# Performance work log

Measured on AMD Instinct MI355X. Metric: run time of the kernel, lower is better.

## Reference

```python
import jax, jax.numpy as jnp
import numpy as np

NUM_TREES = 150
ARITY = 4
DEPTH = 4
NUM_LEVELS = DEPTH + 1  # leaves (level 0) ... root (level DEPTH)
VOCAB = 10000
SUBTOK = 8
EMB_DIM = 256
HID = 256
NUM_CLASSES = 2


def _build_forest():
    # perfect ARITY-ary tree, level-order indexing; edges point child -> parent
    n = (ARITY ** (DEPTH + 1) - 1) // (ARITY - 1)  # 341
    src = np.arange(1, n)
    dst = (src - 1) // ARITY
    depth_of = np.zeros(n, dtype=np.int64)
    for j in range(1, n):
        depth_of[j] = depth_of[(j - 1) // ARITY] + 1
    level_of = DEPTH - depth_of  # leaves = 0, processed first (topo order)
    offs = np.arange(NUM_TREES) * n
    edge_src = (src[None, :] + offs[:, None]).ravel().astype(np.int32)
    edge_dst = (dst[None, :] + offs[:, None]).ravel().astype(np.int32)
    node_level = np.tile(level_of, NUM_TREES).astype(np.int32)
    graph_id = np.repeat(np.arange(NUM_TREES), n).astype(np.int32)
    leaf_mask = (node_level == 0).astype(np.int32)
    return edge_src, edge_dst, node_level, graph_id, leaf_mask, NUM_TREES * n


def setup_inputs() -> dict:
    key = jax.random.key(0)
    ks = jax.random.split(key, 16)
    es, ed, lvl, gid, lm, N = _build_forest()
    s_e = 1.0 / np.sqrt(EMB_DIM)
    s_h = 1.0 / np.sqrt(HID)
    s_f = 1.0 / np.sqrt(2 * HID)
    return {
        "node_feat1": jax.random.randint(ks[0], (N, SUBTOK), 0, VOCAB, dtype=jnp.int32),
        "node_feat2": jax.random.randint(ks[1], (N, SUBTOK), 0, VOCAB, dtype=jnp.int32),
        "emb1": jax.random.normal(ks[2], (VOCAB, EMB_DIM), jnp.float32) * 0.02,
        "emb2": jax.random.normal(ks[3], (VOCAB, EMB_DIM), jnp.float32) * 0.02,
        "W_iou1": jax.random.normal(ks[4], (EMB_DIM, 3 * HID), jnp.float32) * s_e,
        "W_iou2": jax.random.normal(ks[5], (EMB_DIM, 3 * HID), jnp.float32) * s_e,
        "U_iou1": jax.random.normal(ks[6], (HID, 3 * HID), jnp.float32) * s_h,
        "U_iou2": jax.random.normal(ks[7], (HID, 3 * HID), jnp.float32) * s_h,
        "Uf_W1": jax.random.normal(ks[8], (HID, HID), jnp.float32) * s_h,
        "Uf_b1": jnp.zeros((HID,), jnp.float32),
        "Uf_W2": jax.random.normal(ks[9], (HID, HID), jnp.float32) * s_h,
        "Uf_b2": jnp.zeros((HID,), jnp.float32),
        "b_iou1": jnp.zeros((3 * HID,), jnp.float32),
        "b_iou2": jnp.zeros((3 * HID,), jnp.float32),
        "Wf": jax.random.normal(ks[10], (2 * HID, NUM_CLASSES), jnp.float32) * s_f,
        "bf": jnp.zeros((NUM_CLASSES,), jnp.float32),
        "edge_src": jnp.asarray(es),
        "edge_dst": jnp.asarray(ed),
        "node_level": jnp.asarray(lvl),
        "graph_id": jnp.asarray(gid),
        "leaf_mask": jnp.asarray(lm),
    }


def _tree_lstm(iou0, U_iou, Uf_W, Uf_b, b_iou, edge_src, edge_dst, node_level):
    # ChildSum TreeLSTM, propagated level-by-level (leaves -> root)
    N = iou0.shape[0]
    h = jnp.zeros((N, HID), iou0.dtype)
    c = jnp.zeros((N, HID), iou0.dtype)
    for lvl in range(NUM_LEVELS):
        emask = (node_level[edge_dst] == lvl).astype(h.dtype)[:, None]  # [E,1]
        hs = h[edge_src] * emask  # children h (already computed at lower levels)
        f = jax.nn.sigmoid(hs @ Uf_W + Uf_b)  # per-edge forget gate
        h_tild = jax.ops.segment_sum(hs, edge_dst, num_segments=N)
        c_sum = jax.ops.segment_sum(f * c[edge_src] * emask, edge_dst, num_segments=N)
        has_child = jax.ops.segment_sum(emask, edge_dst, num_segments=N) > 0  # [N,1]
        # DGL semantics: reduce overwrites iou for internal nodes; leaves keep W_iou(x)*mask
        iou = jnp.where(has_child, h_tild @ U_iou, iou0) + b_iou
        i, o, u = jnp.split(iou, 3, axis=1)
        c_new = jax.nn.sigmoid(i) * jnp.tanh(u) + c_sum
        h_new = jax.nn.sigmoid(o) * jnp.tanh(c_new)
        at = (node_level == lvl)[:, None]
        h = jnp.where(at, h_new, h)
        c = jnp.where(at, c_new, c)
    return h


def _branch(node_feat, emb, W_iou, U_iou, Uf_W, Uf_b, b_iou,
            leaf_mask, edge_src, edge_dst, node_level, graph_id):
    embeds = emb[node_feat].mean(axis=1)  # subtoken mean pooling -> [N, EMB_DIM]
    iou0 = (embeds @ W_iou) * leaf_mask.astype(embeds.dtype)[:, None]
    h = _tree_lstm(iou0, U_iou, Uf_W, Uf_b, b_iou, edge_src, edge_dst, node_level)
    s = jax.ops.segment_sum(h, graph_id, num_segments=NUM_TREES)
    cnt = jax.ops.segment_sum(jnp.ones((h.shape[0],), h.dtype), graph_id, num_segments=NUM_TREES)
    return jax.nn.relu(s / cnt[:, None])  # mean graph readout + relu


def reference(node_feat1, node_feat2, emb1, emb2, W_iou1, W_iou2, U_iou1, U_iou2,
              Uf_W1, Uf_b1, Uf_W2, Uf_b2, b_iou1, b_iou2, Wf, bf,
              edge_src, edge_dst, node_level, graph_id, leaf_mask):
    m1 = _branch(node_feat1, emb1, W_iou1, U_iou1, Uf_W1, Uf_b1, b_iou1,
                 leaf_mask, edge_src, edge_dst, node_level, graph_id)
    m2 = _branch(node_feat2, emb2, W_iou2, U_iou2, Uf_W2, Uf_b2, b_iou2,
                 leaf_mask, edge_src, edge_dst, node_level, graph_id)
    logits = jax.nn.leaky_relu(jnp.concatenate([m1, m2], axis=1) @ Wf + bf, 0.01)
    return jax.nn.softmax(logits, axis=-1)
```

## Files before the change

### kernel.cpp

```cpp
#include <hip/hip_runtime.h>

#define NT 150
#define NPT 341
#define VOCAB 10000

typedef __attribute__((ext_vector_type(8))) short short8;
typedef __attribute__((ext_vector_type(4))) float floatx4;

__device__ __forceinline__ float sigf(float x){ return 1.0f/(1.0f+__expf(-x)); }
__device__ __forceinline__ float bf2f(ushort u){ union{unsigned i; float f;} v; v.i = ((unsigned)u)<<16; return v.f; }
__device__ __forceinline__ ushort f2bf(float x){ union{float f; unsigned i;} v; v.f = x; return (ushort)((v.i + 0x7fff + ((v.i>>16)&1))>>16); }

__global__ __launch_bounds__(256) void convW_k(
    const float* __restrict__ W1, const float* __restrict__ U1, const float* __restrict__ F1,
    const float* __restrict__ W2, const float* __restrict__ U2, const float* __restrict__ F2,
    ushort* Wt1, ushort* Ut1, ushort* Ft1, ushort* Wt2, ushort* Ut2, ushort* Ft2){
  __shared__ float T[32][33];
  const float* src; ushort* dst; int N;
  switch (blockIdx.z){
    case 0: src=W1; dst=Wt1; N=768; break;
    case 1: src=U1; dst=Ut1; N=768; break;
    case 2: src=F1; dst=Ft1; N=256; break;
    case 3: src=W2; dst=Wt2; N=768; break;
    case 4: src=U2; dst=Ut2; N=768; break;
    default: src=F2; dst=Ft2; N=256; break;
  }
  int n0 = blockIdx.x*32; if (n0 >= N) return;
  int k0 = blockIdx.y*32;
  int nl = threadIdx.x & 31, kb = threadIdx.x >> 5;
  #pragma unroll
  for (int i=0;i<4;i++){ int kk = kb*4+i; T[kk][nl] = src[(size_t)(k0+kk)*N + n0 + nl]; }
  __syncthreads();
  #pragma unroll
  for (int i=0;i<4;i++){ int nn = kb*4+i; dst[(size_t)(n0+nn)*256 + k0 + nl] = f2bf(T[nl][nn]); }
}

__global__ __launch_bounds__(256) void convE_k(
    const float* __restrict__ e1, const float* __restrict__ e2,
    ushort* __restrict__ E1, ushort* __restrict__ E2){
  const float* s = blockIdx.y ? e2 : e1;
  ushort* d = blockIdx.y ? E2 : E1;
  size_t i = ((size_t)blockIdx.x*256 + threadIdx.x)*4;
  float4 v = *(const float4*)&s[i];
  d[i+0]=f2bf(v.x); d[i+1]=f2bf(v.y); d[i+2]=f2bf(v.z); d[i+3]=f2bf(v.w);
}

__global__ __launch_bounds__(1024) void subtree_k(
    const int* __restrict__ f1, const int* __restrict__ f2,
    const ushort* __restrict__ E1, const ushort* __restrict__ E2,
    const ushort* __restrict__ Wt1, const float* __restrict__ b1,
    const ushort* __restrict__ Ut1, const ushort* __restrict__ Ft1, const float* __restrict__ Ufb1,
    const ushort* __restrict__ Wt2, const float* __restrict__ b2,
    const ushort* __restrict__ Ut2, const ushort* __restrict__ Ft2, const float* __restrict__ Ufb2,
    ushort* __restrict__ h1, ushort* __restrict__ c1,
    ushort* __restrict__ h2, ushort* __restrict__ c2,
    float* __restrict__ part){
  __shared__ __attribute__((aligned(16))) ushort As[8][64*40];
  __shared__ __attribute__((aligned(16))) ushort Ht[8][16*40];
  __shared__ float Csum[16][272];
  int br = blockIdx.y;
  const int* feat = br ? f2 : f1;
  const ushort* E = br ? E2 : E1;
  const ushort* Wt = br ? Wt2 : Wt1;
  const float* biou = br ? b2 : b1;
  const ushort* Ut = br ? Ut2 : Ut1;
  const ushort* Ft = br ? Ft2 : Ft1;
  const float* Ufb = br ? Ufb2 : Ufb1;
  ushort* h = br ? h2 : h1;
  ushort* c = br ? c2 : c1;
  int s = blockIdx.x;
  int tree = s >> 2, j = s & 3;
  size_t nbase = (size_t)tree*NPT;
  int tid = threadIdx.x, lane = tid & 63, wav = tid >> 6, quad = lane >> 4, l15 = lane & 15;

  {
    int row = tid >> 4, seg = tid & 15;
    size_t node = nbase + 85 + 64*j + row;
    const int* f = feat + node*8;
    float sm[16];
    #pragma unroll
    for (int q=0;q<16;q++) sm[q]=0.f;
    #pragma unroll
    for (int t8=0;t8<8;t8++){
      const ushort* rp = E + (size_t)f[t8]*256 + seg*16;
      short8 a = *(const short8*)rp;
      short8 b = *(const short8*)(rp+8);
      #pragma unroll
      for (int q=0;q<8;q++){ sm[q]+=bf2f((ushort)a[q]); sm[8+q]+=bf2f((ushort)b[q]); }
    }
    short8 o1, o2;
    #pragma unroll
    for (int q=0;q<8;q++){ o1[q]=(short)f2bf(sm[q]*0.125f); o2[q]=(short)f2bf(sm[8+q]*0.125f); }
    int cch = seg >> 1, off = (seg & 1)*16;
    *(short8*)&As[cch][row*40 + off]     = o1;
    *(short8*)&As[cch][row*40 + off + 8] = o2;
  }
  __syncthreads();

  int hcol = wav*16 + l15;
  int cch = hcol >> 5, coff = hcol & 31;
  float bi = biou[hcol], bo = biou[256+hcol], bu = biou[512+hcol];

  floatx4 acc[3][4];
  #pragma unroll
  for (int g=0;g<3;g++)
    #pragma unroll
    for (int r=0;r<4;r++) acc[g][r] = (floatx4){0.f,0.f,0.f,0.f};
  {
    const ushort* bp0 = Wt + (size_t)(0*256 + hcol)*256 + quad*8;
    const ushort* bp1 = Wt + (size_t)(1*256 + hcol)*256 + quad*8;
    const ushort* bp2 = Wt + (size_t)(2*256 + hcol)*256 + quad*8;
    #pragma unroll
    for (int k8=0;k8<8;k8++){
      short8 b0 = *(const short8*)(bp0 + k8*32);
      short8 b1 = *(const short8*)(bp1 + k8*32);
      short8 b2 = *(const short8*)(bp2 + k8*32);
      #pragma unroll
      for (int r=0;r<4;r++){
        short8 a = *(const short8*)&As[k8][(16*r + l15)*40 + quad*8];
        acc[0][r] = __builtin_amdgcn_mfma_f32_16x16x32_bf16(a, b0, acc[0][r], 0,0,0);
        acc[1][r] = __builtin_amdgcn_mfma_f32_16x16x32_bf16(a, b1, acc[1][r], 0,0,0);
        acc[2][r] = __builtin_amdgcn_mfma_f32_16x16x32_bf16(a, b2, acc[2][r], 0,0,0);
      }
    }
  }
  float hL[4][4], cL[4][4], htd[4];
  #pragma unroll
  for (int r=0;r<4;r++){
    htd[r] = 0.f;
    #pragma unroll
    for (int reg=0;reg<4;reg++){
      float iv = acc[0][r][reg] + bi;
      float ov = acc[1][r][reg] + bo;
      float uv = acc[2][r][reg] + bu;
      float cc_ = sigf(iv)*tanhf(uv);
      float hh = sigf(ov)*tanhf(cc_);
      cL[r][reg] = cc_; hL[r][reg] = hh; htd[r] += hh;
    }
  }
  __syncthreads();
  float sA = 0.f;
  #pragma unroll
  for (int r=0;r<4;r++){
    #pragma unroll
    for (int reg=0;reg<4;reg++){
      As[cch][(16*r + quad*4 + reg)*40 + coff] = f2bf(hL[r][reg]);
      sA += hL[r][reg];
    }
    Ht[cch][(4*r + quad)*40 + coff] = f2bf(htd[r]);
  }
  __syncthreads();

  floatx4 af[4], ai, ao, au;
  #pragma unroll
  for (int r=0;r<4;r++) af[r] = (floatx4){0.f,0.f,0.f,0.f};
  ai = (floatx4){0.f,0.f,0.f,0.f}; ao = ai; au = ai;
  {
    const ushort* bfp = Ft + (size_t)hcol*256 + quad*8;
    const ushort* up0 = Ut + (size_t)(0*256 + hcol)*256 + quad*8;
    const ushort* up1 = Ut + (size_t)(256 + hcol)*256 + quad*8;
    const ushort* up2 = Ut + (size_t)(512 + hcol)*256 + quad*8;
    #pragma unroll
    for (int k8=0;k8<8;k8++){
      short8 Bf = *(const short8*)(bfp + k8*32);
      short8 B0 = *(const short8*)(up0 + k8*32);
      short8 B1 = *(const short8*)(up1 + k8*32);
      short8 B2 = *(const short8*)(up2 + k8*32);
      short8 ah = *(const short8*)&Ht[k8][l15*40 + quad*8];
      #pragma unroll
      for (int r=0;r<4;r++){
        short8 a = *(const short8*)&As[k8][(16*r + l15)*40 + quad*8];
        af[r] = __builtin_amdgcn_mfma_f32_16x16x32_bf16(a, Bf, af[r], 0,0,0);
      }
      ai = __builtin_amdgcn_mfma_f32_16x16x32_bf16(ah, B0, ai, 0,0,0);
      ao = __builtin_amdgcn_mfma_f32_16x16x32_bf16(ah, B1, ao, 0,0,0);
      au = __builtin_amdgcn_mfma_f32_16x16x32_bf16(ah, B2, au, 0,0,0);
    }
  }
  float ufb = Ufb[hcol];
  #pragma unroll
  for (int r=0;r<4;r++){
    float cs = 0.f;
    #pragma unroll
    for (int reg=0;reg<4;reg++) cs += sigf(af[r][reg] + ufb) * cL[r][reg];
    Csum[4*r + quad][hcol] = cs;
  }
  #pragma unroll
  for (int reg=0;reg<4;reg++){
    int p = quad*4 + reg;
    float cs = Csum[p][hcol];
    float iv = ai[reg] + bi, ov = ao[reg] + bo, uv = au[reg] + bu;
    float cn = sigf(iv)*tanhf(uv) + cs;
    float hn = sigf(ov)*tanhf(cn);
    sA += hn;
    size_t off = (nbase + 21 + 16*j + p)*256 + hcol;
    h[off] = f2bf(hn);
    c[off] = f2bf(cn);
  }
  sA += __shfl_xor(sA, 16);
  sA += __shfl_xor(sA, 32);
  if (quad == 0) part[((size_t)(s*2 + br))*256 + hcol] = sA;
}

__global__ __launch_bounds__(1024) void upper_k(
    const ushort* __restrict__ Ut1, const ushort* __restrict__ Ft1,
    const float* __restrict__ Ufb1, const float* __restrict__ b1,
    const ushort* __restrict__ Ut2, const ushort* __restrict__ Ft2,
    const float* __restrict__ Ufb2, const float* __restrict__ b2,
    const ushort* __restrict__ h1, const ushort* __restrict__ c1,
    const ushort* __restrict__ h2, const ushort* __restrict__ c2,
    const float* __restrict__ part, const float* __restrict__ Wf,
    const float* __restrict__ bfv, float* __restrict__ out){
  __shared__ __attribute__((aligned(16))) ushort As[8][64*40];
  __shared__ __attribute__((aligned(16))) ushort Ht[8][16*40];
  __shared__ float Csum[16][272];
  __shared__ float Ms[2][256];
  __shared__ float red[32];
  int tree = blockIdx.x;
  size_t nbase = (size_t)tree*NPT;
  int tid = threadIdx.x, lane = tid & 63, wav = tid >> 6, quad = lane >> 4, l15 = lane & 15;
  int hcol = wav*16 + l15;
  int cch = hcol >> 5, coff = hcol & 31;

  for (int br=0; br<2; br++){
    const ushort* Ut = br ? Ut2 : Ut1;
    const ushort* Ft = br ? Ft2 : Ft1;
    const float* Ufb = br ? Ufb2 : Ufb1;
    const float* biou = br ? b2 : b1;
    const ushort* h = br ? h2 : h1;
    const ushort* c = br ? c2 : c1;
    float bi = biou[hcol], bo = biou[256+hcol], bu = biou[512+hcol];
    float ufb = Ufb[hcol];

    {
      int row = tid >> 4, seg = tid & 15;
      const ushort* src = h + (nbase + 21 + row)*256 + seg*16;
      short8 a = *(const short8*)src;
      short8 b = *(const short8*)(src+8);
      int cc2 = seg >> 1, off = (seg & 1)*16;
      *(short8*)&As[cc2][row*40 + off]     = a;
      *(short8*)&As[cc2][row*40 + off + 8] = b;
    }
    float cL0[4][4];
    #pragma unroll
    for (int r=0;r<4;r++)
      #pragma unroll
      for (int reg=0;reg<4;reg++)
        cL0[r][reg] = bf2f(c[(nbase + 21 + 16*r + quad*4 + reg)*256 + hcol]);
    __syncthreads();
    if (tid < 512){
      int n = tid >> 5, sg = tid & 31;
      int cc2 = sg >> 2, off = (sg & 3)*8;
      float s8[8];
      #pragma unroll
      for (int q=0;q<8;q++) s8[q]=0.f;
      #pragma unroll
      for (int i=0;i<4;i++){
        short8 v = *(const short8*)&As[cc2][(4*n+i)*40 + off];
        #pragma unroll
        for (int q=0;q<8;q++) s8[q] += bf2f((ushort)v[q]);
      }
      short8 o;
      #pragma unroll
      for (int q=0;q<8;q++) o[q] = (short)f2bf(s8[q]);
      *(short8*)&Ht[cc2][n*40 + off] = o;
    }
    __syncthreads();

    const ushort* bfp = Ft + (size_t)hcol*256 + quad*8;
    const ushort* up0 = Ut + (size_t)(0*256 + hcol)*256 + quad*8;
    const ushort* up1 = Ut + (size_t)(256 + hcol)*256 + quad*8;
    const ushort* up2 = Ut + (size_t)(512 + hcol)*256 + quad*8;

    floatx4 af1[4], ai1, ao1, au1;
    #pragma unroll
    for (int r=0;r<4;r++) af1[r] = (floatx4){0.f,0.f,0.f,0.f};
    ai1 = (floatx4){0.f,0.f,0.f,0.f}; ao1 = ai1; au1 = ai1;
    #pragma unroll
    for (int k8=0;k8<8;k8++){
      short8 Bf = *(const short8*)(bfp + k8*32);
      short8 B0 = *(const short8*)(up0 + k8*32);
      short8 B1 = *(const short8*)(up1 + k8*32);
      short8 B2 = *(const short8*)(up2 + k8*32);
      short8 ah = *(const short8*)&Ht[k8][l15*40 + quad*8];
      #pragma unroll
      for (int r=0;r<4;r++){
        short8 a = *(const short8*)&As[k8][(16*r + l15)*40 + quad*8];
        af1[r] = __builtin_amdgcn_mfma_f32_16x16x32_bf16(a, Bf, af1[r], 0,0,0);
      }
      ai1 = __builtin_amdgcn_mfma_f32_16x16x32_bf16(ah, B0, ai1, 0,0,0);
      ao1 = __builtin_amdgcn_mfma_f32_16x16x32_bf16(ah, B1, ao1, 0,0,0);
      au1 = __builtin_amdgcn_mfma_f32_16x16x32_bf16(ah, B2, au1, 0,0,0);
    }
    #pragma unroll
    for (int r=0;r<4;r++){
      float cs = 0.f;
      #pragma unroll
      for (int reg=0;reg<4;reg++) cs += sigf(af1[r][reg] + ufb) * cL0[r][reg];
      Csum[4*r + quad][hcol] = cs;
    }
    float h1v[4], c1v[4], sB = 0.f;
    #pragma unroll
    for (int reg=0;reg<4;reg++){
      int p = quad*4 + reg;
      float cs = Csum[p][hcol];
      float iv = ai1[reg]+bi, ov = ao1[reg]+bo, uv = au1[reg]+bu;
      c1v[reg] = sigf(iv)*tanhf(uv) + cs;
      h1v[reg] = sigf(ov)*tanhf(c1v[reg]);
      sB += h1v[reg];
    }
    __syncthreads();
    #pragma unroll
    for (int reg=0;reg<4;reg++)
      Ht[cch][(quad*4 + reg)*40 + coff] = f2bf(h1v[reg]);
    __syncthreads();

    floatx4 af2, ai2, ao2, au2;
    af2 = (floatx4){0.f,0.f,0.f,0.f}; ai2 = af2; ao2 = af2; au2 = af2;
    #pragma unroll
    for (int k8=0;k8<8;k8++){
      short8 Bf = *(const short8*)(bfp + k8*32);
      short8 B0 = *(const short8*)(up0 + k8*32);
      short8 B1 = *(const short8*)(up1 + k8*32);
      short8 B2 = *(const short8*)(up2 + k8*32);
      short8 a = *(const short8*)&Ht[k8][l15*40 + quad*8];
      af2 = __builtin_amdgcn_mfma_f32_16x16x32_bf16(a, Bf, af2, 0,0,0);
      ai2 = __builtin_amdgcn_mfma_f32_16x16x32_bf16(a, B0, ai2, 0,0,0);
      ao2 = __builtin_amdgcn_mfma_f32_16x16x32_bf16(a, B1, ao2, 0,0,0);
      au2 = __builtin_amdgcn_mfma_f32_16x16x32_bf16(a, B2, au2, 0,0,0);
    }
    float cs2 = 0.f;
    #pragma unroll
    for (int reg=0;reg<4;reg++) cs2 += sigf(af2[reg] + ufb) * c1v[reg];
    float iv2 = ai2[0]+ai2[1]+ai2[2]+ai2[3] + bi;
    float ov2 = ao2[0]+ao2[1]+ao2[2]+ao2[3] + bo;
    float uv2 = au2[0]+au2[1]+au2[2]+au2[3] + bu;
    float c2v = sigf(iv2)*tanhf(uv2) + cs2;
    float h2v = sigf(ov2)*tanhf(c2v);
    sB += h2v;
    __syncthreads();
    Ht[cch][quad*40 + coff] = f2bf(h2v);
    #pragma unroll
    for (int z=1;z<4;z++) Ht[cch][(quad + 4*z)*40 + coff] = 0;
    __syncthreads();

    floatx4 af3, ai3, ao3, au3;
    af3 = (floatx4){0.f,0.f,0.f,0.f}; ai3 = af3; ao3 = af3; au3 = af3;
    #pragma unroll
    for (int k8=0;k8<8;k8++){
      short8 Bf = *(const short8*)(bfp + k8*32);
      short8 B0 = *(const short8*)(up0 + k8*32);
      short8 B1 = *(const short8*)(up1 + k8*32);
      short8 B2 = *(const short8*)(up2 + k8*32);
      short8 a = *(const short8*)&Ht[k8][l15*40 + quad*8];
      af3 = __builtin_amdgcn_mfma_f32_16x16x32_bf16(a, Bf, af3, 0,0,0);
      ai3 = __builtin_amdgcn_mfma_f32_16x16x32_bf16(a, B0, ai3, 0,0,0);
      ao3 = __builtin_amdgcn_mfma_f32_16x16x32_bf16(a, B1, ao3, 0,0,0);
      au3 = __builtin_amdgcn_mfma_f32_16x16x32_bf16(a, B2, au3, 0,0,0);
    }
    float c2c[4];
    #pragma unroll
    for (int reg=0;reg<4;reg++) c2c[reg] = __shfl(c2v, reg*16 + l15);
    {
      float cs3 = 0.f;
      #pragma unroll
      for (int reg=0;reg<4;reg++) cs3 += sigf(af3[reg] + ufb) * c2c[reg];
      float iv3 = ai3[0]+ai3[1]+ai3[2]+ai3[3] + bi;
      float ov3 = ao3[0]+ao3[1]+ao3[2]+ao3[3] + bo;
      float uv3 = au3[0]+au3[1]+au3[2]+au3[3] + bu;
      float c3 = sigf(iv3)*tanhf(uv3) + cs3;
      float hr = sigf(ov3)*tanhf(c3);
      if (quad == 0) sB += hr;
    }
    sB += __shfl_xor(sB, 16);
    sB += __shfl_xor(sB, 32);
    if (quad == 0){
      float tot = sB;
      #pragma unroll
      for (int jj=0;jj<4;jj++)
        tot += part[((size_t)((tree*4 + jj)*2 + br))*256 + hcol];
      Ms[br][hcol] = fmaxf(tot*(1.0f/341.0f), 0.f);
    }
    __syncthreads();
  }

  float p0 = 0.f, p1 = 0.f;
  if (tid < 512){
    float x = Ms[tid >> 8][tid & 255];
    p0 = x*Wf[tid*2+0]; p1 = x*Wf[tid*2+1];
  }
  #pragma unroll
  for (int off=32; off>0; off>>=1){
    p0 += __shfl_down(p0, off);
    p1 += __shfl_down(p1, off);
  }
  if (lane == 0){ red[wav] = p0; red[16+wav] = p1; }
  __syncthreads();
  if (tid == 0){
    float l0 = bfv[0], l1 = bfv[1];
    #pragma unroll
    for (int w=0;w<16;w++){ l0 += red[w]; l1 += red[16+w]; }
    l0 = (l0>0.f)?l0:0.01f*l0;
    l1 = (l1>0.f)?l1:0.01f*l1;
    float mx = fmaxf(l0,l1);
    float e0 = __expf(l0-mx), e1 = __expf(l1-mx);
    float inv = 1.0f/(e0+e1);
    out[tree*2+0] = e0*inv; out[tree*2+1] = e1*inv;
  }
}

extern "C" void kernel_launch(void* const* d_in, const int* in_sizes, int n_in,
                              void* d_out, int out_size, void* d_ws, size_t ws_size,
                              hipStream_t stream) {
  const int*   feat1 = (const int*)  d_in[0];
  const int*   feat2 = (const int*)  d_in[1];
  const float* emb1  = (const float*)d_in[2];
  const float* emb2  = (const float*)d_in[3];
  const float* Wiou1 = (const float*)d_in[4];
  const float* Wiou2 = (const float*)d_in[5];
  const float* Uiou1 = (const float*)d_in[6];
  const float* Uiou2 = (const float*)d_in[7];
  const float* UfW1  = (const float*)d_in[8];
  const float* Ufb1  = (const float*)d_in[9];
  const float* UfW2  = (const float*)d_in[10];
  const float* Ufb2  = (const float*)d_in[11];
  const float* biou1 = (const float*)d_in[12];
  const float* biou2 = (const float*)d_in[13];
  const float* Wf    = (const float*)d_in[14];
  const float* bfv   = (const float*)d_in[15];
  float* out = (float*)d_out;

  char* ws = (char*)d_ws;
  ushort* h1  = (ushort*)ws;  ws += (size_t)NT*NPT*256*2;
  ushort* h2  = (ushort*)ws;  ws += (size_t)NT*NPT*256*2;
  ushort* c1  = (ushort*)ws;  ws += (size_t)NT*NPT*256*2;
  ushort* c2  = (ushort*)ws;  ws += (size_t)NT*NPT*256*2;
  ushort* E1  = (ushort*)ws;  ws += (size_t)VOCAB*256*2;
  ushort* E2  = (ushort*)ws;  ws += (size_t)VOCAB*256*2;
  ushort* Wt1 = (ushort*)ws;  ws += 768*256*2;
  ushort* Ut1 = (ushort*)ws;  ws += 768*256*2;
  ushort* Ft1 = (ushort*)ws;  ws += 256*256*2;
  ushort* Wt2 = (ushort*)ws;  ws += 768*256*2;
  ushort* Ut2 = (ushort*)ws;  ws += 768*256*2;
  ushort* Ft2 = (ushort*)ws;  ws += 256*256*2;
  float*  part = (float*)ws;  ws += (size_t)600*2*256*4;

  convE_k<<<dim3(2500, 2), 256, 0, stream>>>(emb1, emb2, E1, E2);
  convW_k<<<dim3(24, 8, 6), 256, 0, stream>>>(Wiou1, Uiou1, UfW1, Wiou2, Uiou2, UfW2,
                                              Wt1, Ut1, Ft1, Wt2, Ut2, Ft2);
  subtree_k<<<dim3(600, 2), 1024, 0, stream>>>(feat1, feat2, E1, E2,
                                               Wt1, biou1, Ut1, Ft1, Ufb1,
                                               Wt2, biou2, Ut2, Ft2, Ufb2,
                                               h1, c1, h2, c2, part);
  upper_k<<<NT, 1024, 0, stream>>>(Ut1, Ft1, Ufb1, biou1,
                                   Ut2, Ft2, Ufb2, biou2,
                                   h1, c1, h2, c2, part, Wf, bfv, out);
}
```

Measured before the change: 388.9 us.

## Store embedding tables as scaled FP8 and split upper kernel per branch

Embedding tables are now converted to scaled e4m3 FP8 instead of bf16, which halves the bytes moved by the conversion and by the subtoken gather. Separately, the upper-level kernel now runs one block per (tree, branch) instead of looping over both branches, which doubles its parallelism. The classifier head moves into a small final kernel, and subtree blocks interleave the two branches in a 1D grid. FP8 storage lowers embedding precision, and the extra launch adds a small fixed cost.

```diff
diff --git a/kernel.cpp b/kernel.cpp
--- a/kernel.cpp
+++ b/kernel.cpp
@@ -10,6 +10,38 @@
 __device__ __forceinline__ float sigf(float x){ return 1.0f/(1.0f+__expf(-x)); }
 __device__ __forceinline__ float bf2f(ushort u){ union{unsigned i; float f;} v; v.i = ((unsigned)u)<<16; return v.f; }
 __device__ __forceinline__ ushort f2bf(float x){ union{float f; unsigned i;} v; v.f = x; return (ushort)((v.i + 0x7fff + ((v.i>>16)&1))>>16); }
+
+__device__ unsigned char f2e4m3(float x){
+  float a = fabsf(x);
+  unsigned s = (x < 0.f) ? 1u : 0u;
+  if (a != a) return (unsigned char)((s<<7)|0x7f);
+  a = fminf(a, 448.f);
+  unsigned E, M;
+  if (a < 7.8125e-3f){
+    M = (unsigned)rintf(a*512.f); E = 0;
+    if (M > 7){ E = 1; M = 0; }
+  } else {
+    int e; float m = frexpf(a, &e);
+    if (e + 6 <= 0){
+      M = (unsigned)rintf(a*512.f); E = 0;
+      if (M > 7){ E = 1; M = 0; }
+    } else {
+      E = (unsigned)(e + 6);
+      M = (unsigned)rintf((m*2.f - 1.f)*8.f);
+      if (M > 7){ M = 0; E++; }
+      if (E > 15){ E = 15; M = 6; }
+    }
+  }
+  return (unsigned char)((s<<7)|(E<<3)|M);
+}
+
+__device__ __forceinline__ float fp8d(unsigned b){
+  unsigned e = (b>>3)&15u, m = b&7u, t = (e==0u) ? 1u : 0u;
+  union{unsigned u; float f;} w;
+  w.u = ((e + 120u + t)<<23) | (m<<20);
+  float mag = w.f - (t ? 0.015625f : 0.f);
+  return (b & 0x80u) ? -mag : mag;
+}
 
 __global__ __launch_bounds__(256) void convW_k(
     const float* __restrict__ W1, const float* __restrict__ U1, const float* __restrict__ F1,
@@ -37,17 +69,20 @@
 
 __global__ __launch_bounds__(256) void convE_k(
     const float* __restrict__ e1, const float* __restrict__ e2,
-    ushort* __restrict__ E1, ushort* __restrict__ E2){
+    unsigned char* __restrict__ E1, unsigned char* __restrict__ E2){
   const float* s = blockIdx.y ? e2 : e1;
-  ushort* d = blockIdx.y ? E2 : E1;
+  unsigned char* d = blockIdx.y ? E2 : E1;
   size_t i = ((size_t)blockIdx.x*256 + threadIdx.x)*4;
   float4 v = *(const float4*)&s[i];
-  d[i+0]=f2bf(v.x); d[i+1]=f2bf(v.y); d[i+2]=f2bf(v.z); d[i+3]=f2bf(v.w);
+  uchar4 o;
+  o.x = f2e4m3(v.x*64.f); o.y = f2e4m3(v.y*64.f);
+  o.z = f2e4m3(v.z*64.f); o.w = f2e4m3(v.w*64.f);
+  *(uchar4*)&d[i] = o;
 }
 
 __global__ __launch_bounds__(1024) void subtree_k(
     const int* __restrict__ f1, const int* __restrict__ f2,
-    const ushort* __restrict__ E1, const ushort* __restrict__ E2,
+    const unsigned char* __restrict__ E1, const unsigned char* __restrict__ E2,
     const ushort* __restrict__ Wt1, const float* __restrict__ b1,
     const ushort* __restrict__ Ut1, const ushort* __restrict__ Ft1, const float* __restrict__ Ufb1,
     const ushort* __restrict__ Wt2, const float* __restrict__ b2,
@@ -58,9 +93,11 @@
   __shared__ __attribute__((aligned(16))) ushort As[8][64*40];
   __shared__ __attribute__((aligned(16))) ushort Ht[8][16*40];
   __shared__ float Csum[16][272];
-  int br = blockIdx.y;
+  int bid = blockIdx.x;
+  int br = bid & 1;
+  int s = bid >> 1;
   const int* feat = br ? f2 : f1;
-  const ushort* E = br ? E2 : E1;
+  const unsigned char* E = br ? E2 : E1;
   const ushort* Wt = br ? Wt2 : Wt1;
   const float* biou = br ? b2 : b1;
   const ushort* Ut = br ? Ut2 : Ut1;
@@ -68,7 +105,6 @@
   const float* Ufb = br ? Ufb2 : Ufb1;
   ushort* h = br ? h2 : h1;
   ushort* c = br ? c2 : c1;
-  int s = blockIdx.x;
   int tree = s >> 2, j = s & 3;
   size_t nbase = (size_t)tree*NPT;
   int tid = threadIdx.x, lane = tid & 63, wav = tid >> 6, quad = lane >> 4, l15 = lane & 15;
@@ -82,15 +118,20 @@
     for (int q=0;q<16;q++) sm[q]=0.f;
     #pragma unroll
     for (int t8=0;t8<8;t8++){
-      const ushort* rp = E + (size_t)f[t8]*256 + seg*16;
-      short8 a = *(const short8*)rp;
-      short8 b = *(const short8*)(rp+8);
+      uint4 rv = *(const uint4*)(E + (size_t)f[t8]*256 + seg*16);
+      unsigned wd[4] = {rv.x, rv.y, rv.z, rv.w};
       #pragma unroll
-      for (int q=0;q<8;q++){ sm[q]+=bf2f((ushort)a[q]); sm[8+q]+=bf2f((ushort)b[q]); }
+      for (int w=0;w<4;w++)
+        #pragma unroll
+        for (int b8=0;b8<4;b8++)
+          sm[w*4+b8] += fp8d((wd[w]>>(8*b8)) & 0xffu);
     }
     short8 o1, o2;
     #pragma unroll
-    for (int q=0;q<8;q++){ o1[q]=(short)f2bf(sm[q]*0.125f); o2[q]=(short)f2bf(sm[8+q]*0.125f); }
+    for (int q=0;q<8;q++){
+      o1[q]=(short)f2bf(sm[q]*0.001953125f);
+      o2[q]=(short)f2bf(sm[8+q]*0.001953125f);
+    }
     int cch = seg >> 1, off = (seg & 1)*16;
     *(short8*)&As[cch][row*40 + off]     = o1;
     *(short8*)&As[cch][row*40 + off + 8] = o2;
@@ -209,197 +250,195 @@
     const float* __restrict__ Ufb2, const float* __restrict__ b2,
     const ushort* __restrict__ h1, const ushort* __restrict__ c1,
     const ushort* __restrict__ h2, const ushort* __restrict__ c2,
-    const float* __restrict__ part, const float* __restrict__ Wf,
-    const float* __restrict__ bfv, float* __restrict__ out){
+    const float* __restrict__ part,
+    float* __restrict__ m1, float* __restrict__ m2){
   __shared__ __attribute__((aligned(16))) ushort As[8][64*40];
   __shared__ __attribute__((aligned(16))) ushort Ht[8][16*40];
   __shared__ float Csum[16][272];
-  __shared__ float Ms[2][256];
-  __shared__ float red[32];
-  int tree = blockIdx.x;
+  int bid = blockIdx.x;
+  int br = bid & 1;
+  int tree = bid >> 1;
+  const ushort* Ut = br ? Ut2 : Ut1;
+  const ushort* Ft = br ? Ft2 : Ft1;
+  const float* Ufb = br ? Ufb2 : Ufb1;
+  const float* biou = br ? b2 : b1;
+  const ushort* h = br ? h2 : h1;
+  const ushort* c = br ? c2 : c1;
+  float* mo = br ? m2 : m1;
   size_t nbase = (size_t)tree*NPT;
   int tid = threadIdx.x, lane = tid & 63, wav = tid >> 6, quad = lane >> 4, l15 = lane & 15;
   int hcol = wav*16 + l15;
   int cch = hcol >> 5, coff = hcol & 31;
-
-  for (int br=0; br<2; br++){
-    const ushort* Ut = br ? Ut2 : Ut1;
-    const ushort* Ft = br ? Ft2 : Ft1;
-    const float* Ufb = br ? Ufb2 : Ufb1;
-    const float* biou = br ? b2 : b1;
-    const ushort* h = br ? h2 : h1;
-    const ushort* c = br ? c2 : c1;
-    float bi = biou[hcol], bo = biou[256+hcol], bu = biou[512+hcol];
-    float ufb = Ufb[hcol];
-
-    {
-      int row = tid >> 4, seg = tid & 15;
-      const ushort* src = h + (nbase + 21 + row)*256 + seg*16;
-      short8 a = *(const short8*)src;
-      short8 b = *(const short8*)(src+8);
-      int cc2 = seg >> 1, off = (seg & 1)*16;
-      *(short8*)&As[cc2][row*40 + off]     = a;
-      *(short8*)&As[cc2][row*40 + off + 8] = b;
-    }
-    float cL0[4][4];
-    #pragma unroll
-    for (int r=0;r<4;r++)
+  float bi = biou[hcol], bo = biou[256+hcol], bu = biou[512+hcol];
+  float ufb = Ufb[hcol];
+
+  {
+    int row = tid >> 4, seg = tid & 15;
+    const ushort* src = h + (nbase + 21 + row)*256 + seg*16;
+    short8 a = *(const short8*)src;
+    short8 b = *(const short8*)(src+8);
+    int cc2 = seg >> 1, off = (seg & 1)*16;
+    *(short8*)&As[cc2][row*40 + off]     = a;
+    *(short8*)&As[cc2][row*40 + off + 8] = b;
+  }
+  float cL0[4][4];
+  #pragma unroll
+  for (int r=0;r<4;r++)
+    #pragma unroll
+    for (int reg=0;reg<4;reg++)
+      cL0[r][reg] = bf2f(c[(nbase + 21 + 16*r + quad*4 + reg)*256 + hcol]);
+  __syncthreads();
+  if (tid < 512){
+    int n = tid >> 5, sg = tid & 31;
+    int cc2 = sg >> 2, off = (sg & 3)*8;
+    float s8[8];
+    #pragma unroll
+    for (int q=0;q<8;q++) s8[q]=0.f;
+    #pragma unroll
+    for (int i=0;i<4;i++){
+      short8 v = *(const short8*)&As[cc2][(4*n+i)*40 + off];
       #pragma unroll
-      for (int reg=0;reg<4;reg++)
-        cL0[r][reg] = bf2f(c[(nbase + 21 + 16*r + quad*4 + reg)*256 + hcol]);
-    __syncthreads();
-    if (tid < 512){
-      int n = tid >> 5, sg = tid & 31;
-      int cc2 = sg >> 2, off = (sg & 3)*8;
-      float s8[8];
-      #pragma unroll
-      for (int q=0;q<8;q++) s8[q]=0.f;
-      #pragma unroll
-      for (int i=0;i<4;i++){
-        short8 v = *(const short8*)&As[cc2][(4*n+i)*40 + off];
-        #pragma unroll
-        for (int q=0;q<8;q++) s8[q] += bf2f((ushort)v[q]);
-      }
-      short8 o;
-      #pragma unroll
-      for (int q=0;q<8;q++) o[q] = (short)f2bf(s8[q]);
-      *(short8*)&Ht[cc2][n*40 + off] = o;
-    }
-    __syncthreads();
-
-    const ushort* bfp = Ft + (size_t)hcol*256 + quad*8;
-    const ushort* up0 = Ut + (size_t)(0*256 + hcol)*256 + quad*8;
-    const ushort* up1 = Ut + (size_t)(256 + hcol)*256 + quad*8;
-    const ushort* up2 = Ut + (size_t)(512 + hcol)*256 + quad*8;
-
-    floatx4 af1[4], ai1, ao1, au1;
-    #pragma unroll
-    for (int r=0;r<4;r++) af1[r] = (floatx4){0.f,0.f,0.f,0.f};
-    ai1 = (floatx4){0.f,0.f,0.f,0.f}; ao1 = ai1; au1 = ai1;
-    #pragma unroll
-    for (int k8=0;k8<8;k8++){
-      short8 Bf = *(const short8*)(bfp + k8*32);
-      short8 B0 = *(const short8*)(up0 + k8*32);
-      short8 B1 = *(const short8*)(up1 + k8*32);
-      short8 B2 = *(const short8*)(up2 + k8*32);
-      short8 ah = *(const short8*)&Ht[k8][l15*40 + quad*8];
-      #pragma unroll
-      for (int r=0;r<4;r++){
-        short8 a = *(const short8*)&As[k8][(16*r + l15)*40 + quad*8];
-        af1[r] = __builtin_amdgcn_mfma_f32_16x16x32_bf16(a, Bf, af1[r], 0,0,0);
-      }
-      ai1 = __builtin_amdgcn_mfma_f32_16x16x32_bf16(ah, B0, ai1, 0,0,0);
-      ao1 = __builtin_amdgcn_mfma_f32_16x16x32_bf16(ah, B1, ao1, 0,0,0);
-      au1 = __builtin_amdgcn_mfma_f32_16x16x32_bf16(ah, B2, au1, 0,0,0);
-    }
+      for (int q=0;q<8;q++) s8[q] += bf2f((ushort)v[q]);
+    }
+    short8 o;
+    #pragma unroll
+    for (int q=0;q<8;q++) o[q] = (short)f2bf(s8[q]);
+    *(short8*)&Ht[cc2][n*40 + off] = o;
+  }
+  __syncthreads();
+
+  const ushort* bfp = Ft + (size_t)hcol*256 + quad*8;
+  const ushort* up0 = Ut + (size_t)(0*256 + hcol)*256 + quad*8;
+  const ushort* up1 = Ut + (size_t)(256 + hcol)*256 + quad*8;
+  const ushort* up2 = Ut + (size_t)(512 + hcol)*256 + quad*8;
+
+  floatx4 af1[4], ai1, ao1, au1;
+  #pragma unroll
+  for (int r=0;r<4;r++) af1[r] = (floatx4){0.f,0.f,0.f,0.f};
+  ai1 = (floatx4){0.f,0.f,0.f,0.f}; ao1 = ai1; au1 = ai1;
+  #pragma unroll
+  for (int k8=0;k8<8;k8++){
+    short8 Bf = *(const short8*)(bfp + k8*32);
+    short8 B0 = *(const short8*)(up0 + k8*32);
+    short8 B1 = *(const short8*)(up1 + k8*32);
+    short8 B2 = *(const short8*)(up2 + k8*32);
+    short8 ah = *(const short8*)&Ht[k8][l15*40 + quad*8];
     #pragma unroll
     for (int r=0;r<4;r++){
-      float cs = 0.f;
-      #pragma unroll
-      for (int reg=0;reg<4;reg++) cs += sigf(af1[r][reg] + ufb) * cL0[r][reg];
-      Csum[4*r + quad][hcol] = cs;
-    }
-    float h1v[4], c1v[4], sB = 0.f;
-    #pragma unroll
-    for (int reg=0;reg<4;reg++){
-      int p = quad*4 + reg;
-      float cs = Csum[p][hcol];
-      float iv = ai1[reg]+bi, ov = ao1[reg]+bo, uv = au1[reg]+bu;
-      c1v[reg] = sigf(iv)*tanhf(uv) + cs;
-      h1v[reg] = sigf(ov)*tanhf(c1v[reg]);
-      sB += h1v[reg];
-    }
-    __syncthreads();
-    #pragma unroll
-    for (int reg=0;reg<4;reg++)
-      Ht[cch][(quad*4 + reg)*40 + coff] = f2bf(h1v[reg]);
-    __syncthreads();
-
-    floatx4 af2, ai2, ao2, au2;
-    af2 = (floatx4){0.f,0.f,0.f,0.f}; ai2 = af2; ao2 = af2; au2 = af2;
-    #pragma unroll
-    for (int k8=0;k8<8;k8++){
-      short8 Bf = *(const short8*)(bfp + k8*32);
-      short8 B0 = *(const short8*)(up0 + k8*32);
-      short8 B1 = *(const short8*)(up1 + k8*32);
-      short8 B2 = *(const short8*)(up2 + k8*32);
-      short8 a = *(const short8*)&Ht[k8][l15*40 + quad*8];
-      af2 = __builtin_amdgcn_mfma_f32_16x16x32_bf16(a, Bf, af2, 0,0,0);
-      ai2 = __builtin_amdgcn_mfma_f32_16x16x32_bf16(a, B0, ai2, 0,0,0);
-      ao2 = __builtin_amdgcn_mfma_f32_16x16x32_bf16(a, B1, ao2, 0,0,0);
-      au2 = __builtin_amdgcn_mfma_f32_16x16x32_bf16(a, B2, au2, 0,0,0);
-    }
-    float cs2 = 0.f;
-    #pragma unroll
-    for (int reg=0;reg<4;reg++) cs2 += sigf(af2[reg] + ufb) * c1v[reg];
-    float iv2 = ai2[0]+ai2[1]+ai2[2]+ai2[3] + bi;
-    float ov2 = ao2[0]+ao2[1]+ao2[2]+ao2[3] + bo;
-    float uv2 = au2[0]+au2[1]+au2[2]+au2[3] + bu;
-    float c2v = sigf(iv2)*tanhf(uv2) + cs2;
-    float h2v = sigf(ov2)*tanhf(c2v);
-    sB += h2v;
-    __syncthreads();
-    Ht[cch][quad*40 + coff] = f2bf(h2v);
-    #pragma unroll
-    for (int z=1;z<4;z++) Ht[cch][(quad + 4*z)*40 + coff] = 0;
-    __syncthreads();
-
-    floatx4 af3, ai3, ao3, au3;
-    af3 = (floatx4){0.f,0.f,0.f,0.f}; ai3 = af3; ao3 = af3; au3 = af3;
-    #pragma unroll
-    for (int k8=0;k8<8;k8++){
-      short8 Bf = *(const short8*)(bfp + k8*32);
-      short8 B0 = *(const short8*)(up0 + k8*32);
-      short8 B1 = *(const short8*)(up1 + k8*32);
-      short8 B2 = *(const short8*)(up2 + k8*32);
-      short8 a = *(const short8*)&Ht[k8][l15*40 + quad*8];
-      af3 = __builtin_amdgcn_mfma_f32_16x16x32_bf16(a, Bf, af3, 0,0,0);
-      ai3 = __builtin_amdgcn_mfma_f32_16x16x32_bf16(a, B0, ai3, 0,0,0);
-      ao3 = __builtin_amdgcn_mfma_f32_16x16x32_bf16(a, B1, ao3, 0,0,0);
-      au3 = __builtin_amdgcn_mfma_f32_16x16x32_bf16(a, B2, au3, 0,0,0);
-    }
-    float c2c[4];
-    #pragma unroll
-    for (int reg=0;reg<4;reg++) c2c[reg] = __shfl(c2v, reg*16 + l15);
-    {
-      float cs3 = 0.f;
-      #pragma unroll
-      for (int reg=0;reg<4;reg++) cs3 += sigf(af3[reg] + ufb) * c2c[reg];
-      float iv3 = ai3[0]+ai3[1]+ai3[2]+ai3[3] + bi;
-      float ov3 = ao3[0]+ao3[1]+ao3[2]+ao3[3] + bo;
-      float uv3 = au3[0]+au3[1]+au3[2]+au3[3] + bu;
-      float c3 = sigf(iv3)*tanhf(uv3) + cs3;
-      float hr = sigf(ov3)*tanhf(c3);
-      if (quad == 0) sB += hr;
-    }
-    sB += __shfl_xor(sB, 16);
-    sB += __shfl_xor(sB, 32);
-    if (quad == 0){
-      float tot = sB;
-      #pragma unroll
-      for (int jj=0;jj<4;jj++)
-        tot += part[((size_t)((tree*4 + jj)*2 + br))*256 + hcol];
-      Ms[br][hcol] = fmaxf(tot*(1.0f/341.0f), 0.f);
-    }
-    __syncthreads();
-  }
-
-  float p0 = 0.f, p1 = 0.f;
-  if (tid < 512){
-    float x = Ms[tid >> 8][tid & 255];
-    p0 = x*Wf[tid*2+0]; p1 = x*Wf[tid*2+1];
+      short8 a = *(const short8*)&As[k8][(16*r + l15)*40 + quad*8];
+      af1[r] = __builtin_amdgcn_mfma_f32_16x16x32_bf16(a, Bf, af1[r], 0,0,0);
+    }
+    ai1 = __builtin_amdgcn_mfma_f32_16x16x32_bf16(ah, B0, ai1, 0,0,0);
+    ao1 = __builtin_amdgcn_mfma_f32_16x16x32_bf16(ah, B1, ao1, 0,0,0);
+    au1 = __builtin_amdgcn_mfma_f32_16x16x32_bf16(ah, B2, au1, 0,0,0);
+  }
+  #pragma unroll
+  for (int r=0;r<4;r++){
+    float cs = 0.f;
+    #pragma unroll
+    for (int reg=0;reg<4;reg++) cs += sigf(af1[r][reg] + ufb) * cL0[r][reg];
+    Csum[4*r + quad][hcol] = cs;
+  }
+  float h1v[4], c1v[4], sB = 0.f;
+  #pragma unroll
+  for (int reg=0;reg<4;reg++){
+    int p = quad*4 + reg;
+    float cs = Csum[p][hcol];
+    float iv = ai1[reg]+bi, ov = ao1[reg]+bo, uv = au1[reg]+bu;
+    c1v[reg] = sigf(iv)*tanhf(uv) + cs;
+    h1v[reg] = sigf(ov)*tanhf(c1v[reg]);
+    sB += h1v[reg];
+  }
+  __syncthreads();
+  #pragma unroll
+  for (int reg=0;reg<4;reg++)
+    Ht[cch][(quad*4 + reg)*40 + coff] = f2bf(h1v[reg]);
+  __syncthreads();
+
+  floatx4 af2, ai2, ao2, au2;
+  af2 = (floatx4){0.f,0.f,0.f,0.f}; ai2 = af2; ao2 = af2; au2 = af2;
+  #pragma unroll
+  for (int k8=0;k8<8;k8++){
+    short8 Bf = *(const short8*)(bfp + k8*32);
+    short8 B0 = *(const short8*)(up0 + k8*32);
+    short8 B1 = *(const short8*)(up1 + k8*32);
+    short8 B2 = *(const short8*)(up2 + k8*32);
+    short8 a = *(const short8*)&Ht[k8][l15*40 + quad*8];
+    af2 = __builtin_amdgcn_mfma_f32_16x16x32_bf16(a, Bf, af2, 0,0,0);
+    ai2 = __builtin_amdgcn_mfma_f32_16x16x32_bf16(a, B0, ai2, 0,0,0);
+    ao2 = __builtin_amdgcn_mfma_f32_16x16x32_bf16(a, B1, ao2, 0,0,0);
+    au2 = __builtin_amdgcn_mfma_f32_16x16x32_bf16(a, B2, au2, 0,0,0);
+  }
+  float cs2 = 0.f;
+  #pragma unroll
+  for (int reg=0;reg<4;reg++) cs2 += sigf(af2[reg] + ufb) * c1v[reg];
+  float iv2 = ai2[0]+ai2[1]+ai2[2]+ai2[3] + bi;
+  float ov2 = ao2[0]+ao2[1]+ao2[2]+ao2[3] + bo;
+  float uv2 = au2[0]+au2[1]+au2[2]+au2[3] + bu;
+  float c2v = sigf(iv2)*tanhf(uv2) + cs2;
+  float h2v = sigf(ov2)*tanhf(c2v);
+  sB += h2v;
+  __syncthreads();
+  Ht[cch][quad*40 + coff] = f2bf(h2v);
+  #pragma unroll
+  for (int z=1;z<4;z++) Ht[cch][(quad + 4*z)*40 + coff] = 0;
+  __syncthreads();
+
+  floatx4 af3, ai3, ao3, au3;
+  af3 = (floatx4){0.f,0.f,0.f,0.f}; ai3 = af3; ao3 = af3; au3 = af3;
+  #pragma unroll
+  for (int k8=0;k8<8;k8++){
+    short8 Bf = *(const short8*)(bfp + k8*32);
+    short8 B0 = *(const short8*)(up0 + k8*32);
+    short8 B1 = *(const short8*)(up1 + k8*32);
+    short8 B2 = *(const short8*)(up2 + k8*32);
+    short8 a = *(const short8*)&Ht[k8][l15*40 + quad*8];
+    af3 = __builtin_amdgcn_mfma_f32_16x16x32_bf16(a, Bf, af3, 0,0,0);
+    ai3 = __builtin_amdgcn_mfma_f32_16x16x32_bf16(a, B0, ai3, 0,0,0);
+    ao3 = __builtin_amdgcn_mfma_f32_16x16x32_bf16(a, B1, ao3, 0,0,0);
+    au3 = __builtin_amdgcn_mfma_f32_16x16x32_bf16(a, B2, au3, 0,0,0);
+  }
+  float c2c[4];
+  #pragma unroll
+  for (int reg=0;reg<4;reg++) c2c[reg] = __shfl(c2v, reg*16 + l15);
+  {
+    float cs3 = 0.f;
+    #pragma unroll
+    for (int reg=0;reg<4;reg++) cs3 += sigf(af3[reg] + ufb) * c2c[reg];
+    float iv3 = ai3[0]+ai3[1]+ai3[2]+ai3[3] + bi;
+    float ov3 = ao3[0]+ao3[1]+ao3[2]+ao3[3] + bo;
+    float uv3 = au3[0]+au3[1]+au3[2]+au3[3] + bu;
+    float c3 = sigf(iv3)*tanhf(uv3) + cs3;
+    float hr = sigf(ov3)*tanhf(c3);
+    if (quad == 0) sB += hr;
+  }
+  sB += __shfl_xor(sB, 16);
+  sB += __shfl_xor(sB, 32);
+  if (quad == 0){
+    float tot = sB;
+    #pragma unroll
+    for (int jj=0;jj<4;jj++)
+      tot += part[((size_t)((tree*4 + jj)*2 + br))*256 + hcol];
+    mo[tree*256 + hcol] = fmaxf(tot*(1.0f/341.0f), 0.f);
+  }
+}
+
+__global__ __launch_bounds__(64) void final_k(const float* __restrict__ m1,
+    const float* __restrict__ m2, const float* __restrict__ Wf,
+    const float* __restrict__ bf, float* __restrict__ out){
+  int tree = blockIdx.x; int t = threadIdx.x;
+  float p0=0.f, p1=0.f;
+  for (int k=t;k<512;k+=64){
+    float x = (k<256) ? m1[tree*256+k] : m2[tree*256+(k-256)];
+    p0 += x*Wf[k*2+0]; p1 += x*Wf[k*2+1];
   }
   #pragma unroll
   for (int off=32; off>0; off>>=1){
     p0 += __shfl_down(p0, off);
     p1 += __shfl_down(p1, off);
   }
-  if (lane == 0){ red[wav] = p0; red[16+wav] = p1; }
-  __syncthreads();
-  if (tid == 0){
-    float l0 = bfv[0], l1 = bfv[1];
-    #pragma unroll
-    for (int w=0;w<16;w++){ l0 += red[w]; l1 += red[16+w]; }
+  if (t==0){
+    float l0 = p0+bf[0], l1 = p1+bf[1];
     l0 = (l0>0.f)?l0:0.01f*l0;
     l1 = (l1>0.f)?l1:0.01f*l1;
     float mx = fmaxf(l0,l1);
@@ -435,8 +474,8 @@
   ushort* h2  = (ushort*)ws;  ws += (size_t)NT*NPT*256*2;
   ushort* c1  = (ushort*)ws;  ws += (size_t)NT*NPT*256*2;
   ushort* c2  = (ushort*)ws;  ws += (size_t)NT*NPT*256*2;
-  ushort* E1  = (ushort*)ws;  ws += (size_t)VOCAB*256*2;
-  ushort* E2  = (ushort*)ws;  ws += (size_t)VOCAB*256*2;
+  unsigned char* E1 = (unsigned char*)ws;  ws += (size_t)VOCAB*256;
+  unsigned char* E2 = (unsigned char*)ws;  ws += (size_t)VOCAB*256;
   ushort* Wt1 = (ushort*)ws;  ws += 768*256*2;
   ushort* Ut1 = (ushort*)ws;  ws += 768*256*2;
   ushort* Ft1 = (ushort*)ws;  ws += 256*256*2;
@@ -444,15 +483,18 @@
   ushort* Ut2 = (ushort*)ws;  ws += 768*256*2;
   ushort* Ft2 = (ushort*)ws;  ws += 256*256*2;
   float*  part = (float*)ws;  ws += (size_t)600*2*256*4;
+  float*  m1  = (float*)ws;   ws += (size_t)NT*256*4;
+  float*  m2  = (float*)ws;   ws += (size_t)NT*256*4;
 
   convE_k<<<dim3(2500, 2), 256, 0, stream>>>(emb1, emb2, E1, E2);
   convW_k<<<dim3(24, 8, 6), 256, 0, stream>>>(Wiou1, Uiou1, UfW1, Wiou2, Uiou2, UfW2,
                                               Wt1, Ut1, Ft1, Wt2, Ut2, Ft2);
-  subtree_k<<<dim3(600, 2), 1024, 0, stream>>>(feat1, feat2, E1, E2,
-                                               Wt1, biou1, Ut1, Ft1, Ufb1,
-                                               Wt2, biou2, Ut2, Ft2, Ufb2,
-                                               h1, c1, h2, c2, part);
-  upper_k<<<NT, 1024, 0, stream>>>(Ut1, Ft1, Ufb1, biou1,
-                                   Ut2, Ft2, Ufb2, biou2,
-                                   h1, c1, h2, c2, part, Wf, bfv, out);
-}
+  subtree_k<<<1200, 1024, 0, stream>>>(feat1, feat2, E1, E2,
+                                       Wt1, biou1, Ut1, Ft1, Ufb1,
+                                       Wt2, biou2, Ut2, Ft2, Ufb2,
+                                       h1, c1, h2, c2, part);
+  upper_k<<<300, 1024, 0, stream>>>(Ut1, Ft1, Ufb1, biou1,
+                                    Ut2, Ft2, Ufb2, biou2,
+                                    h1, c1, h2, c2, part, m1, m2);
+  final_k<<<NT, 64, 0, stream>>>(m1, m2, Wf, bfv, out);
+}
```

New measurement: 418.0 us. 1.08x slower.
